# Kernel tuning notes

Hardware: AMD Instinct MI355X
Metric: run time of the kernel (lower is better)

The kernel has to match this reference:

```python
import jax, jax.numpy as jnp
import numpy as np

B, T, D, H = 4, 1024, 1024, 16
DK = D // H
SCALE = float(np.sqrt(DK))


def setup_inputs() -> dict:
    key = jax.random.key(0)
    ks = jax.random.split(key, 12)
    std = 1.0 / np.sqrt(D)
    inp = {
        "x": jax.random.normal(ks[0], (B, T, D), dtype=jnp.float32),
        "s2_distances": jax.random.uniform(ks[1], (B, T, T), dtype=jnp.float32),
        # causal mask: 1 where attention allowed (j <= i)
        "mask": jnp.broadcast_to(jnp.tril(jnp.ones((T, T), dtype=jnp.int32)), (B, T, T)),
        "Wq": jax.random.uniform(ks[2], (D, D), jnp.float32, -std, std),
        "bq": jax.random.uniform(ks[3], (D,), jnp.float32, -std, std),
        "Wk": jax.random.uniform(ks[4], (D, D), jnp.float32, -std, std),
        "bk": jax.random.uniform(ks[5], (D,), jnp.float32, -std, std),
        "Wv": jax.random.uniform(ks[6], (D, D), jnp.float32, -std, std),
        "bv": jax.random.uniform(ks[7], (D,), jnp.float32, -std, std),
        "Wo": jax.random.uniform(ks[8], (D, D), jnp.float32, -std, std),
        "bo": jax.random.uniform(ks[9], (D,), jnp.float32, -std, std),
        "spatial_weight": jnp.float32(0.5),
    }
    return inp


def reference(x, s2_distances, mask, Wq, bq, Wk, bk, Wv, bv, Wo, bo, spatial_weight):
    b, t, _ = x.shape
    # projections: torch nn.Linear is x @ W.T + b
    def proj(W, bias):
        y = jnp.einsum("btd,ed->bte", x, W) + bias
        return y.reshape(b, t, H, DK).transpose(0, 2, 1, 3)  # [B,H,T,dk]

    Q, K, V = proj(Wq, bq), proj(Wk, bk), proj(Wv, bv)
    # scores: QK^T/sqrt(dk) - |alpha| * dist  (dist broadcast over heads)
    scores = jnp.einsum("bhqd,bhkd->bhqk", Q, K) / SCALE
    scores = scores - jnp.abs(spatial_weight) * s2_distances[:, None, :, :]
    scores = jnp.where(mask[:, None, :, :] == 0, -jnp.inf, scores)
    probs = jax.nn.softmax(scores, axis=-1)
    out = jnp.einsum("bhqk,bhkd->bhqd", probs, V)
    out = out.transpose(0, 2, 1, 3).reshape(b, t, D)
    return jnp.einsum("btd,ed->bte", out, Wo) + bo
```

## Files before the change

### kernel.cpp

```cpp
#include <hip/hip_runtime.h>
#include <stdint.h>

#define Tt 1024
#define Dd 1024
#define Hh 16

typedef unsigned short u16;
typedef __attribute__((ext_vector_type(8))) short short8;
typedef __attribute__((ext_vector_type(4))) float f32x4;
typedef __attribute__((ext_vector_type(4))) unsigned short u16x4;

typedef const __attribute__((address_space(1))) uint32_t* gptr_t;
typedef __attribute__((address_space(3))) uint32_t* lptr_t;

#define QSCALE 0.18033688011112042f
#define LOG2E 1.4426950408889634f

static __device__ __forceinline__ u16 f2bf(float f) {
  union { float f; unsigned u; } x;
  x.f = f;
  unsigned u = x.u;
  return (u16)((u + 0x7fffu + ((u >> 16) & 1u)) >> 16);
}

static __device__ __forceinline__ u16 f2bf_fast(float f) {
  union { float f; unsigned u; } x;
  x.f = f;
  return (u16)((x.u + 0x8000u) >> 16);
}

static __device__ __forceinline__ float bf2f(u16 u) {
  union { unsigned u; float f; } x;
  x.u = ((unsigned)u) << 16;
  return x.f;
}

static __device__ __forceinline__ float fexp2(float x) {
#if __has_builtin(__builtin_amdgcn_exp2f)
  return __builtin_amdgcn_exp2f(x);
#else
  return exp2f(x);
#endif
}

__global__ __launch_bounds__(256) void cvt_kernel(
    const float* __restrict__ x, const float* __restrict__ wq,
    const float* __restrict__ wk, const float* __restrict__ wv,
    const float* __restrict__ wo, u16* __restrict__ xb, u16* __restrict__ wb) {
  size_t i = ((size_t)blockIdx.x * 256 + threadIdx.x) * 4;
  const size_t XN = (size_t)4 * 1024 * 1024;
  const float* src;
  u16* dst;
  size_t off;
  if (i < XN) {
    src = x; dst = xb; off = i;
  } else {
    size_t j = i - XN;
    int wi = (int)(j >> 20);
    src = (wi == 0) ? wq : (wi == 1) ? wk : (wi == 2) ? wv : wo;
    dst = wb + ((size_t)wi << 20);
    off = j & ((1u << 20) - 1);
  }
  float4 v = *(const float4*)(src + off);
  u16x4 o;
  o.x = f2bf(v.x); o.y = f2bf(v.y); o.z = f2bf(v.z); o.w = f2bf(v.w);
  *(u16x4*)(dst + off) = o;
}

__global__ __launch_bounds__(512, 2) void qkv_fused_kernel(
    const u16* __restrict__ xb, const u16* __restrict__ wb,
    const float* __restrict__ bq, const float* __restrict__ bk,
    const float* __restrict__ bv, u16* __restrict__ Q, u16* __restrict__ Kk,
    u16* __restrict__ Vt, const float* __restrict__ dist,
    const float* __restrict__ alphap, u16* __restrict__ biasb) {
  __shared__ u16 lds[65536];
  const int bid = blockIdx.x;
  if (bid >= 192) {
    const int cid = bid - 192;
    const float scl = -fabsf(alphap[0]) * LOG2E;
    const size_t id = (size_t)cid * 512 + threadIdx.x;
#pragma unroll 4
    for (int i = 0; i < 32; i++) {
      const size_t off = id * 4 + (size_t)i * 131072;
      float4 v = *(const float4*)(dist + off);
      u16x4 o;
      o.x = f2bf(v.x * scl); o.y = f2bf(v.y * scl);
      o.z = f2bf(v.z * scl); o.w = f2bf(v.w * scl);
      *(u16x4*)(biasb + off) = o;
    }
    return;
  }
  const int mt = bid & 15, ny = bid >> 4;
  const int z = ny >> 2;
  const int m0 = mt * 256, nc = (ny & 3) * 256;
  const u16* W = wb + ((size_t)z << 20);

  const int t = threadIdx.x, w = t >> 6, l = t & 63;
  const int quad = l >> 4, l15 = l & 15;
  const int wr = w >> 2, wn = w & 3;
  char* ldc = (char*)lds;

  const int srow = w * 16 + ((l >> 3) & 7);
  const int schunk = ((l & 7) ^ ((l >> 3) & 7)) * 8;
  const u16* gA = xb + (size_t)(m0 + srow) * Dd + schunk;
  const u16* gB = W + (size_t)(nc + srow) * Dd + schunk;

  auto stage = [&](int kt, int h) {
    const size_t ro = (size_t)(h * 128) * Dd + (size_t)kt * 64;
    char* base = ldc + ((((kt & 1) << 1) | h) * 32768) + w * 2048;
#pragma unroll
    for (int i = 0; i < 2; i++) {
      __builtin_amdgcn_global_load_lds((gptr_t)(gA + ro + (size_t)i * 8 * Dd),
                                       (lptr_t)(base + i * 1024), 16, 0, 0);
      __builtin_amdgcn_global_load_lds((gptr_t)(gB + ro + (size_t)i * 8 * Dd),
                                       (lptr_t)(base + 16384 + i * 1024), 16, 0, 0);
    }
  };

  f32x4 acc[8][4];
#pragma unroll
  for (int i = 0; i < 8; i++)
#pragma unroll
    for (int j = 0; j < 4; j++) acc[i][j] = (f32x4){0.f, 0.f, 0.f, 0.f};

  stage(0, 0); stage(0, 1);
  stage(1, 0); stage(1, 1);
  asm volatile("s_waitcnt vmcnt(8)" ::: "memory");
  __builtin_amdgcn_s_barrier();

  const int swl = l15 & 7;

#pragma unroll 1
  for (int kt = 0; kt < 16; kt++) {
    const char* slA = ldc + ((((kt & 1) << 1) | wr) * 32768);
    const char* slB = ldc + ((((kt & 1) << 1) | (wn >> 1)) * 32768) + 16384;
    const int rB = (wn & 1) * 64;
    {
      short8 af[8], bfv[4];
      const int cs = ((0 * 4 + quad) ^ swl) * 16;
#pragma unroll
      for (int mi = 0; mi < 8; mi++)
        af[mi] = *(const short8*)(slA + (mi * 16 + l15) * 128 + cs);
#pragma unroll
      for (int ni = 0; ni < 4; ni++)
        bfv[ni] = *(const short8*)(slB + (rB + ni * 16 + l15) * 128 + cs);
      __builtin_amdgcn_s_barrier();
      asm volatile("s_waitcnt lgkmcnt(0)" ::: "memory");
      __builtin_amdgcn_sched_barrier(0);
      __builtin_amdgcn_s_setprio(1);
#pragma unroll
      for (int mi = 0; mi < 8; mi++)
#pragma unroll
        for (int ni = 0; ni < 4; ni++)
          acc[mi][ni] = __builtin_amdgcn_mfma_f32_16x16x32_bf16(
              af[mi], bfv[ni], acc[mi][ni], 0, 0, 0);
      __builtin_amdgcn_s_setprio(0);
    }
    {
      short8 af[8], bfv[4];
      const int cs = ((1 * 4 + quad) ^ swl) * 16;
#pragma unroll
      for (int mi = 0; mi < 8; mi++)
        af[mi] = *(const short8*)(slA + (mi * 16 + l15) * 128 + cs);
#pragma unroll
      for (int ni = 0; ni < 4; ni++)
        bfv[ni] = *(const short8*)(slB + (rB + ni * 16 + l15) * 128 + cs);
      __builtin_amdgcn_s_barrier();
      if (kt + 2 < 16) { stage(kt + 2, 0); stage(kt + 2, 1); }
      asm volatile("s_waitcnt lgkmcnt(0)" ::: "memory");
      __builtin_amdgcn_sched_barrier(0);
      __builtin_amdgcn_s_setprio(1);
#pragma unroll
      for (int mi = 0; mi < 8; mi++)
#pragma unroll
        for (int ni = 0; ni < 4; ni++)
          acc[mi][ni] = __builtin_amdgcn_mfma_f32_16x16x32_bf16(
              af[mi], bfv[ni], acc[mi][ni], 0, 0, 0);
      __builtin_amdgcn_s_setprio(0);
      if (kt < 14) {
        asm volatile("s_waitcnt vmcnt(8)" ::: "memory");
      } else if (kt == 14) {
        asm volatile("s_waitcnt vmcnt(0)" ::: "memory");
      }
      if (kt < 15) __builtin_amdgcn_s_barrier();
    }
  }

  const float* bias = (z == 0) ? bq : (z == 1) ? bk : bv;
  const float scl = (z == 0) ? QSCALE : 1.0f;
  if (z < 2) {
#pragma unroll
    for (int mi = 0; mi < 8; mi++)
#pragma unroll
      for (int ni = 0; ni < 4; ni++) {
        const int n = wn * 64 + ni * 16 + l15;
        const float bn = bias[nc + n];
        const int nsw = n ^ (quad << 4);
#pragma unroll
        for (int r = 0; r < 4; r++) {
          const int m = wr * 128 + mi * 16 + quad * 4 + r;
          lds[m * 256 + nsw] = f2bf((acc[mi][ni][r] + bn) * scl);
        }
      }
  } else {
#pragma unroll
    for (int mi = 0; mi < 8; mi++)
#pragma unroll
      for (int ni = 0; ni < 4; ni++) {
        const int n = wn * 64 + ni * 16 + l15;
        const float bn = bias[nc + n];
        u16x4 o;
        o.x = f2bf(acc[mi][ni][0] + bn);
        o.y = f2bf(acc[mi][ni][1] + bn);
        o.z = f2bf(acc[mi][ni][2] + bn);
        o.w = f2bf(acc[mi][ni][3] + bn);
        const int mp = (wr * 128 + mi * 16 + quad * 4) ^ ((n & 7) * 8);
        *(u16x4*)&lds[n * 256 + mp] = o;
      }
  }
  __syncthreads();
  const int row = t >> 5;
  const int c8 = (t & 31) * 8;
  if (z < 2) {
    u16* out = (z == 0) ? Q : Kk;
#pragma unroll
    for (int it = 0; it < 16; it++) {
      const int rr = it * 16 + row;
      const int pos = c8 ^ ((((rr >> 2) & 3)) << 4);
      *(short8*)(out + (size_t)(m0 + rr) * Dd + nc + c8) =
          *(const short8*)&lds[rr * 256 + pos];
    }
  } else {
    const int b2 = m0 >> 10, t0 = m0 & (Tt - 1);
#pragma unroll
    for (int it = 0; it < 16; it++) {
      const int rr = it * 16 + row;
      const int pos = c8 ^ ((rr & 7) * 8);
      *(short8*)(Vt + ((size_t)b2 * Dd + nc + rr) * Tt + t0 + c8) =
          *(const short8*)&lds[rr * 256 + pos];
    }
  }
}

__global__ __launch_bounds__(512) void gemm_out_kernel(
    const u16* __restrict__ Ao, const u16* __restrict__ Wo,
    const float* __restrict__ bo, float* __restrict__ out) {
  __shared__ u16 lds[32768];
  const int mt = blockIdx.x & 31, ny = blockIdx.x >> 5;
  const int m0 = mt * 128, n0 = ny * 128;
  const int t = threadIdx.x, w = t >> 6, l = t & 63;
  const int quad = l >> 4, l15 = l & 15;
  const int wr = w >> 2, wn = w & 3;
  char* ldc = (char*)lds;

  const int srow = w * 8 + (l >> 3);
  const int schunk = ((l & 7) ^ ((l >> 3) & 7)) * 8;
  const u16* gA = Ao + (size_t)(m0 + srow) * Dd + schunk;
  const u16* gB = Wo + (size_t)(n0 + srow) * Dd + schunk;

  auto stage = [&](int kt) {
    char* base = ldc + (kt & 1) * 32768 + w * 1024;
#pragma unroll
    for (int i = 0; i < 2; i++) {
      __builtin_amdgcn_global_load_lds(
          (gptr_t)(gA + (size_t)i * 64 * Dd + (size_t)kt * 64),
          (lptr_t)(base + i * 8192), 16, 0, 0);
      __builtin_amdgcn_global_load_lds(
          (gptr_t)(gB + (size_t)i * 64 * Dd + (size_t)kt * 64),
          (lptr_t)(base + 16384 + i * 8192), 16, 0, 0);
    }
  };

  f32x4 acc[4][2];
#pragma unroll
  for (int i = 0; i < 4; i++)
#pragma unroll
    for (int j = 0; j < 2; j++) acc[i][j] = (f32x4){0.f, 0.f, 0.f, 0.f};

  stage(0); stage(1);
  asm volatile("s_waitcnt vmcnt(4)" ::: "memory");
  __builtin_amdgcn_s_barrier();

  const int swl = l15 & 7;

#pragma unroll 1
  for (int kt = 0; kt < 16; kt++) {
    const char* sl = ldc + (kt & 1) * 32768;
    short8 af[2][4], bfv[2][2];
#pragma unroll
    for (int ks = 0; ks < 2; ks++) {
      const int cs = ((ks * 4 + quad) ^ swl) * 16;
#pragma unroll
      for (int mi = 0; mi < 4; mi++)
        af[ks][mi] = *(const short8*)(sl + (wr * 64 + mi * 16 + l15) * 128 + cs);
#pragma unroll
      for (int ni = 0; ni < 2; ni++)
        bfv[ks][ni] = *(const short8*)(sl + 16384 + (wn * 32 + ni * 16 + l15) * 128 + cs);
    }
    __builtin_amdgcn_s_barrier();
    if (kt + 2 < 16) stage(kt + 2);
    asm volatile("s_waitcnt lgkmcnt(0)" ::: "memory");
    __builtin_amdgcn_sched_barrier(0);
    __builtin_amdgcn_s_setprio(1);
#pragma unroll
    for (int ks = 0; ks < 2; ks++)
#pragma unroll
      for (int mi = 0; mi < 4; mi++)
#pragma unroll
        for (int ni = 0; ni < 2; ni++)
          acc[mi][ni] = __builtin_amdgcn_mfma_f32_16x16x32_bf16(
              af[ks][mi], bfv[ks][ni], acc[mi][ni], 0, 0, 0);
    __builtin_amdgcn_s_setprio(0);
    if (kt < 14) {
      asm volatile("s_waitcnt vmcnt(4)" ::: "memory");
    } else if (kt == 14) {
      asm volatile("s_waitcnt vmcnt(0)" ::: "memory");
    }
    if (kt < 15) __builtin_amdgcn_s_barrier();
  }

#pragma unroll
  for (int mi = 0; mi < 4; mi++)
#pragma unroll
    for (int ni = 0; ni < 2; ni++) {
      const int n = n0 + wn * 32 + ni * 16 + l15;
      const float bn = bo[n];
#pragma unroll
      for (int r = 0; r < 4; r++) {
        const int m = m0 + wr * 64 + mi * 16 + quad * 4 + r;
        out[(size_t)m * Dd + n] = acc[mi][ni][r] + bn;
      }
    }
}

__global__ __launch_bounds__(256) void attn_kernel(
    const u16* __restrict__ Q, const u16* __restrict__ Kk,
    const u16* __restrict__ Vt, const u16* __restrict__ biasb,
    u16* __restrict__ Oo) {
  __shared__ u16 lK[2][64 * 64];
  __shared__ u16 lV[2][64 * 64];
  __shared__ u16 lPp[4][16 * 64];
  const int t = threadIdx.x, w = t >> 6, l = t & 63, quad = l >> 4, l15 = l & 15;
  const int g = blockIdx.x >> 8;
  const int j = (blockIdx.x >> 6) & 3;
  const int bh = blockIdx.x & 63;
  const int qb = (g == 0) ? 15 - j : (g == 1) ? 8 + j : (g == 2) ? 7 - j : j;
  const int h = bh & (Hh - 1), b = bh >> 4;
  const int q0 = qb * 64;

  const int srow = w * 8 + (l >> 3);
  const int schunk = ((l & 7) ^ ((l >> 3) & 7)) * 8;
  const u16* gK = Kk + ((size_t)b * Tt + srow) * Dd + h * 64 + schunk;
  const u16* gV = Vt + ((size_t)b * Dd + h * 64 + srow) * Tt + schunk;
  char* lKc0 = (char*)&lK[0][0];
  char* lVc0 = (char*)&lV[0][0];
  const int wbase = w * 1024;

  auto stage = [&](int k0, int buf) {
#pragma unroll
    for (int i = 0; i < 2; i++) {
      __builtin_amdgcn_global_load_lds(
          (gptr_t)(gK + (size_t)(k0 + i * 32) * Dd),
          (lptr_t)(lKc0 + buf * 8192 + wbase + i * 4096), 16, 0, 0);
      __builtin_amdgcn_global_load_lds(
          (gptr_t)(gV + (size_t)(i * 32) * Tt + k0),
          (lptr_t)(lVc0 + buf * 8192 + wbase + i * 4096), 16, 0, 0);
    }
  };

  const int qrow = q0 + w * 16 + l15;
  const u16* Qp = Q + ((size_t)b * Tt + qrow) * Dd + h * 64 + quad * 8;
  const short8 qf0 = *(const short8*)Qp;
  const short8 qf1 = *(const short8*)(Qp + 32);
  const u16* bp = biasb + ((size_t)b * Tt + qrow) * Tt + quad * 4;

  const int xr = l15 & 7;
  u16* lpr = &lPp[w][l15 * 64];
  const int niter = qb + 1;

  f32x4 oacc[4];
#pragma unroll
  for (int dt = 0; dt < 4; dt++) oacc[dt] = (f32x4){0.f, 0.f, 0.f, 0.f};
  f32x4 lsum4 = (f32x4){0.f, 0.f, 0.f, 0.f};
  u16x4 bbA[4], bbB[4];

  stage(0, 0);
#pragma unroll
  for (int nt = 0; nt < 4; nt++) bbA[nt] = *(const u16x4*)(bp + nt * 16);

#pragma unroll 1
  for (int kt = 0; kt < niter; kt++) {
    const int buf = kt & 1;
    __builtin_amdgcn_s_waitcnt(0);
    __syncthreads();
    if (kt + 1 < niter) {
      stage((kt + 1) * 64, buf ^ 1);
#pragma unroll
      for (int nt = 0; nt < 4; nt++)
        bbB[nt] = *(const u16x4*)(bp + (kt + 1) * 64 + nt * 16);
    }
    f32x4 sacc[4];
#pragma unroll
    for (int nt = 0; nt < 4; nt++) {
#pragma unroll
      for (int r = 0; r < 4; r++) sacc[nt][r] = bf2f(bbA[nt][r]);
    }
#pragma unroll
    for (int ks = 0; ks < 2; ks++) {
      const short8 qf = ks ? qf1 : qf0;
      const int cs = ((ks * 4 + quad) ^ xr) * 8;
#pragma unroll
      for (int nt = 0; nt < 4; nt++) {
        const short8 kf = *(const short8*)&lK[buf][(nt * 16 + l15) * 64 + cs];
        sacc[nt] = __builtin_amdgcn_mfma_f32_16x16x32_bf16(kf, qf, sacc[nt], 0, 0, 0);
      }
    }
    if (kt == qb) {
      const int kbase = kt * 64 + quad * 4;
#pragma unroll
      for (int nt = 0; nt < 4; nt++) {
        u16x4 pk;
#pragma unroll
        for (int r = 0; r < 4; r++) {
          const float p = (kbase + nt * 16 + r <= qrow) ? fexp2(sacc[nt][r]) : 0.f;
          lsum4[nt] += p;
          pk[r] = f2bf_fast(p);
        }
        *(u16x4*)&lpr[((nt * 4 + quad) ^ (xr << 1)) * 4] = pk;
      }
    } else {
#pragma unroll
      for (int nt = 0; nt < 4; nt++) {
        u16x4 pk;
#pragma unroll
        for (int r = 0; r < 4; r++) {
          const float p = fexp2(sacc[nt][r]);
          lsum4[nt] += p;
          pk[r] = f2bf_fast(p);
        }
        *(u16x4*)&lpr[((nt * 4 + quad) ^ (xr << 1)) * 4] = pk;
      }
    }
#pragma unroll
    for (int ks = 0; ks < 2; ks++) {
      const int cs = ((ks * 4 + quad) ^ xr) * 8;
      const short8 pa = *(const short8*)&lpr[cs];
#pragma unroll
      for (int dt = 0; dt < 4; dt++) {
        const short8 vf = *(const short8*)&lV[buf][(dt * 16 + l15) * 64 + cs];
        oacc[dt] = __builtin_amdgcn_mfma_f32_16x16x32_bf16(pa, vf, oacc[dt], 0, 0, 0);
      }
    }
#pragma unroll
    for (int nt = 0; nt < 4; nt++) bbA[nt] = bbB[nt];
  }

  float lsum = (lsum4[0] + lsum4[1]) + (lsum4[2] + lsum4[3]);
  lsum += __shfl_xor(lsum, 16);
  lsum += __shfl_xor(lsum, 32);
  const float inv = 1.0f / lsum;
  float invq[4];
#pragma unroll
  for (int r = 0; r < 4; r++) invq[r] = __shfl(inv, quad * 4 + r);
#pragma unroll
  for (int dt = 0; dt < 4; dt++) {
#pragma unroll
    for (int r = 0; r < 4; r++) {
      Oo[((size_t)b * Tt + q0 + w * 16 + quad * 4 + r) * Dd + h * 64 + dt * 16 + l15] =
          f2bf(oacc[dt][r] * invq[r]);
    }
  }
}

extern "C" void kernel_launch(void* const* d_in, const int* in_sizes, int n_in,
                              void* d_out, int out_size, void* d_ws, size_t ws_size,
                              hipStream_t stream) {
  const float* x = (const float*)d_in[0];
  const float* dist = (const float*)d_in[1];
  const float* Wq = (const float*)d_in[3];
  const float* bq = (const float*)d_in[4];
  const float* Wk = (const float*)d_in[5];
  const float* bk = (const float*)d_in[6];
  const float* Wv = (const float*)d_in[7];
  const float* bv = (const float*)d_in[8];
  const float* Wo = (const float*)d_in[9];
  const float* bo = (const float*)d_in[10];
  const float* alphap = (const float*)d_in[11];

  char* ws = (char*)d_ws;
  u16* xb = (u16*)(ws);
  u16* wb = (u16*)(ws + ((size_t)8 << 20));
  u16* Qb = (u16*)(ws + ((size_t)16 << 20));
  u16* Kb = (u16*)(ws + ((size_t)24 << 20));
  u16* Vtb = (u16*)(ws + ((size_t)32 << 20));
  u16* biasb = (u16*)(ws + ((size_t)40 << 20));
  u16* Ob = xb;
  float* outp = (float*)d_out;

  cvt_kernel<<<8192, 256, 0, stream>>>(x, Wq, Wk, Wv, Wo, xb, wb);
  qkv_fused_kernel<<<256, 512, 0, stream>>>(xb, wb, bq, bk, bv, Qb, Kb, Vtb,
                                            dist, alphap, biasb);
  attn_kernel<<<1024, 256, 0, stream>>>(Qb, Kb, Vtb, biasb, Ob);
  gemm_out_kernel<<<256, 512, 0, stream>>>(Ob, wb + ((size_t)3 << 20), bo, outp);
}
```

Measured before the change: 192.7 us.

## Read fp32 distances directly in attention, drop bf16 bias precompute pass

```diff
diff --git a/kernel.cpp b/kernel.cpp
--- a/kernel.cpp
+++ b/kernel.cpp
@@ -27,12 +27,6 @@
   union { float f; unsigned u; } x;
   x.f = f;
   return (u16)((x.u + 0x8000u) >> 16);
-}
-
-static __device__ __forceinline__ float bf2f(u16 u) {
-  union { unsigned u; float f; } x;
-  x.u = ((unsigned)u) << 16;
-  return x.f;
 }
 
 static __device__ __forceinline__ float fexp2(float x) {
@@ -71,25 +65,9 @@
     const u16* __restrict__ xb, const u16* __restrict__ wb,
     const float* __restrict__ bq, const float* __restrict__ bk,
     const float* __restrict__ bv, u16* __restrict__ Q, u16* __restrict__ Kk,
-    u16* __restrict__ Vt, const float* __restrict__ dist,
-    const float* __restrict__ alphap, u16* __restrict__ biasb) {
+    u16* __restrict__ Vt) {
   __shared__ u16 lds[65536];
   const int bid = blockIdx.x;
-  if (bid >= 192) {
-    const int cid = bid - 192;
-    const float scl = -fabsf(alphap[0]) * LOG2E;
-    const size_t id = (size_t)cid * 512 + threadIdx.x;
-#pragma unroll 4
-    for (int i = 0; i < 32; i++) {
-      const size_t off = id * 4 + (size_t)i * 131072;
-      float4 v = *(const float4*)(dist + off);
-      u16x4 o;
-      o.x = f2bf(v.x * scl); o.y = f2bf(v.y * scl);
-      o.z = f2bf(v.z * scl); o.w = f2bf(v.w * scl);
-      *(u16x4*)(biasb + off) = o;
-    }
-    return;
-  }
   const int mt = bid & 15, ny = bid >> 4;
   const int z = ny >> 2;
   const int m0 = mt * 256, nc = (ny & 3) * 256;
@@ -335,8 +313,8 @@
 
 __global__ __launch_bounds__(256) void attn_kernel(
     const u16* __restrict__ Q, const u16* __restrict__ Kk,
-    const u16* __restrict__ Vt, const u16* __restrict__ biasb,
-    u16* __restrict__ Oo) {
+    const u16* __restrict__ Vt, const float* __restrict__ dist,
+    const float* __restrict__ alphap, u16* __restrict__ Oo) {
   __shared__ u16 lK[2][64 * 64];
   __shared__ u16 lV[2][64 * 64];
   __shared__ u16 lPp[4][16 * 64];
@@ -347,6 +325,7 @@
   const int qb = (g == 0) ? 15 - j : (g == 1) ? 8 + j : (g == 2) ? 7 - j : j;
   const int h = bh & (Hh - 1), b = bh >> 4;
   const int q0 = qb * 64;
+  const float scl = -fabsf(alphap[0]) * LOG2E;
 
   const int srow = w * 8 + (l >> 3);
   const int schunk = ((l & 7) ^ ((l >> 3) & 7)) * 8;
@@ -372,7 +351,7 @@
   const u16* Qp = Q + ((size_t)b * Tt + qrow) * Dd + h * 64 + quad * 8;
   const short8 qf0 = *(const short8*)Qp;
   const short8 qf1 = *(const short8*)(Qp + 32);
-  const u16* bp = biasb + ((size_t)b * Tt + qrow) * Tt + quad * 4;
+  const float* bp = dist + ((size_t)b * Tt + qrow) * Tt + quad * 4;
 
   const int xr = l15 & 7;
   u16* lpr = &lPp[w][l15 * 64];
@@ -382,28 +361,39 @@
 #pragma unroll
   for (int dt = 0; dt < 4; dt++) oacc[dt] = (f32x4){0.f, 0.f, 0.f, 0.f};
   f32x4 lsum4 = (f32x4){0.f, 0.f, 0.f, 0.f};
-  u16x4 bbA[4], bbB[4];
+  f32x4 bbA[4], bbB[4], bbC[4];
 
   stage(0, 0);
 #pragma unroll
-  for (int nt = 0; nt < 4; nt++) bbA[nt] = *(const u16x4*)(bp + nt * 16);
+  for (int nt = 0; nt < 4; nt++) bbA[nt] = *(const f32x4*)(bp + nt * 16);
+  if (niter > 1) {
+#pragma unroll
+    for (int nt = 0; nt < 4; nt++) bbB[nt] = *(const f32x4*)(bp + 64 + nt * 16);
+  } else {
+#pragma unroll
+    for (int nt = 0; nt < 4; nt++) bbB[nt] = bbA[nt];
+  }
 
 #pragma unroll 1
   for (int kt = 0; kt < niter; kt++) {
     const int buf = kt & 1;
-    __builtin_amdgcn_s_waitcnt(0);
-    __syncthreads();
     if (kt + 1 < niter) {
-      stage((kt + 1) * 64, buf ^ 1);
+      asm volatile("s_waitcnt vmcnt(4)" ::: "memory");
+    } else {
+      asm volatile("s_waitcnt vmcnt(0)" ::: "memory");
+    }
+    __builtin_amdgcn_s_barrier();
+    if (kt + 1 < niter) stage((kt + 1) * 64, buf ^ 1);
+    if (kt + 2 < niter) {
 #pragma unroll
       for (int nt = 0; nt < 4; nt++)
-        bbB[nt] = *(const u16x4*)(bp + (kt + 1) * 64 + nt * 16);
+        bbC[nt] = *(const f32x4*)(bp + (kt + 2) * 64 + nt * 16);
     }
     f32x4 sacc[4];
 #pragma unroll
     for (int nt = 0; nt < 4; nt++) {
 #pragma unroll
-      for (int r = 0; r < 4; r++) sacc[nt][r] = bf2f(bbA[nt][r]);
+      for (int r = 0; r < 4; r++) sacc[nt][r] = scl * bbA[nt][r];
     }
 #pragma unroll
     for (int ks = 0; ks < 2; ks++) {
@@ -452,7 +442,7 @@
       }
     }
 #pragma unroll
-    for (int nt = 0; nt < 4; nt++) bbA[nt] = bbB[nt];
+    for (int nt = 0; nt < 4; nt++) { bbA[nt] = bbB[nt]; bbB[nt] = bbC[nt]; }
   }
 
   float lsum = (lsum4[0] + lsum4[1]) + (lsum4[2] + lsum4[3]);
@@ -493,13 +483,11 @@
   u16* Qb = (u16*)(ws + ((size_t)16 << 20));
   u16* Kb = (u16*)(ws + ((size_t)24 << 20));
   u16* Vtb = (u16*)(ws + ((size_t)32 << 20));
-  u16* biasb = (u16*)(ws + ((size_t)40 << 20));
   u16* Ob = xb;
   float* outp = (float*)d_out;
 
   cvt_kernel<<<8192, 256, 0, stream>>>(x, Wq, Wk, Wv, Wo, xb, wb);
-  qkv_fused_kernel<<<256, 512, 0, stream>>>(xb, wb, bq, bk, bv, Qb, Kb, Vtb,
-                                            dist, alphap, biasb);
-  attn_kernel<<<1024, 256, 0, stream>>>(Qb, Kb, Vtb, biasb, Ob);
+  qkv_fused_kernel<<<192, 512, 0, stream>>>(xb, wb, bq, bk, bv, Qb, Kb, Vtb);
+  attn_kernel<<<1024, 256, 0, stream>>>(Qb, Kb, Vtb, dist, alphap, Ob);
   gemm_out_kernel<<<256, 512, 0, stream>>>(Ob, wb + ((size_t)3 << 20), bo, outp);
 }
```

Measured after the change: 198.9 us. 1.03x slower.
